# Kernel tuning notes

Hardware: AMD Instinct MI355X
Metric: run time of the kernel (lower is better)

Reference implementation:

```python
import jax, jax.numpy as jnp
import numpy as np

N, D, H = 65536, 512, 256  # batch, input_dim, hidden_dim
BN_EPS = 1e-5
EPS = 1e-15


def setup_inputs() -> dict:
    key = jax.random.key(0)
    ks = jax.random.split(key, 10)
    rn = lambda k, shape, sc: jax.random.normal(k, shape, dtype=jnp.float32) * sc
    return {
        "x1": rn(ks[0], (N, D), 1.0),
        "x2": rn(ks[1], (N, D), 1.0),
        "W1": rn(ks[2], (D, H), 0.04),
        "b1": jnp.zeros((H,), jnp.float32),
        "gamma": jnp.ones((H,), jnp.float32),
        "beta_bn": jnp.zeros((H,), jnp.float32),
        "W2": rn(ks[3], (H, H // 2), 0.06),
        "b2": jnp.zeros((H // 2,), jnp.float32),
        "W3": rn(ks[4], (H // 2 * 3, 64), 0.05),
        "b3": jnp.zeros((64,), jnp.float32),
        "W4": rn(ks[5], (64, 1), 0.12),
        "b4": jnp.zeros((1,), jnp.float32),
        "alpha": jnp.array([0.65], jnp.float32),
        "beta": jnp.array([0.25], jnp.float32),
    }


def _proj(x, W1, b1, gamma, beta_bn, W2, b2):
    h = x @ W1 + b1                       # [N, 256]
    mean = jnp.mean(h, axis=0)
    var = jnp.var(h, axis=0)              # biased, matches BN training normalization
    h = gamma * (h - mean) * jax.lax.rsqrt(var + BN_EPS) + beta_bn
    h = jax.nn.relu(h)
    return jax.nn.relu(h @ W2 + b2)       # [N, 128]


def reference(x1, x2, W1, b1, gamma, beta_bn, W2, b2, W3, b3, W4, b4, alpha, beta):
    h1 = _proj(x1, W1, b1, gamma, beta_bn, W2, b2)
    h2 = _proj(x2, W1, b1, gamma, beta_bn, W2, b2)
    # diag of normalized similarity matrix == row-wise cosine similarity
    dot = jnp.sum(h1 * h2, axis=1)
    inv1 = 1.0 / jnp.maximum(jnp.sqrt(jnp.sum(h1 * h1, axis=1)), EPS)
    inv2 = 1.0 / jnp.maximum(jnp.sqrt(jnp.sum(h2 * h2, axis=1)), EPS)
    s_math = jnp.clip(dot * inv1 * inv2, 0.0, 1.0)
    combined = jnp.concatenate([h1 * h2, jnp.abs(h1 - h2), h1 + h2], axis=1)  # [N, 384]
    s_learn = (jax.nn.relu(combined @ W3 + b3) @ W4 + b4).reshape(-1)          # [N]
    final = alpha * s_math + beta * jax.nn.sigmoid(s_learn)
    return jnp.clip(final, 0.0, 1.0)
```

## Files before the change

kernel.cpp:

```cpp
#include <hip/hip_runtime.h>
#include <hip/hip_bf16.h>
#include <math.h>

#define NROWS 65536
#define DIN   512
#define H1    256
#define H2    128
#define K3DIM 384
#define O3    64

typedef short  short8  __attribute__((ext_vector_type(8)));
typedef float  f32x4   __attribute__((ext_vector_type(4)));
typedef unsigned short u16x4 __attribute__((ext_vector_type(4)));

__device__ __forceinline__ unsigned short f2bf(float f) {
    union { float f; unsigned int i; } v; v.f = f;
    unsigned int r = (v.i + 0x7fffu + ((v.i >> 16) & 1u)) >> 16;
    return (unsigned short)r;
}
__device__ __forceinline__ float bf2f(unsigned short u) {
    union { unsigned int i; float f; } v; v.i = ((unsigned int)u) << 16;
    return v.f;
}

typedef const __attribute__((address_space(1))) unsigned int* gas1_t;
typedef __attribute__((address_space(3))) unsigned int* las3_t;
__device__ __forceinline__ void gload_lds16(const void* g, void* l) {
    __builtin_amdgcn_global_load_lds((gas1_t)g, (las3_t)l, 16, 0, 0);
}

__global__ void transpose_cvt_kernel(const float* __restrict__ src,
                                     unsigned short* __restrict__ dst, int R, int C) {
    int idx = blockIdx.x * 256 + threadIdx.x;
    if (idx >= R * C) return;
    int c = idx / R, r = idx - c * R;
    dst[idx] = f2bf(src[r * C + c]);
}

#define LDA1 32

__global__ __launch_bounds__(256, 2)
void gemm1_kernel(const float* __restrict__ x1, const float* __restrict__ x2,
                  const unsigned short* __restrict__ w1t, const float* __restrict__ b1,
                  unsigned short* __restrict__ h_out, float* __restrict__ stats) {
    __shared__ __align__(1024) unsigned short Al[64 * LDA1];
    __shared__ __align__(1024) unsigned short Bl[256 * LDA1];
    const int t    = threadIdx.x;
    const int row0 = blockIdx.x * 64;
    const int inp  = row0 >> 16;
    const float* xp = inp ? x2 : x1;
    const int r0 = row0 & (NROWS - 1);

    const int wave = t >> 6, lane = t & 63;
    const int m = lane & 15, q = lane >> 4;

    const int bn_local = lane >> 2;
    const int bk_off   = (lane & 3) * 8;

    f32x4 acc[4][4] = {};

    for (int k0 = 0; k0 < DIN; k0 += 32) {
        __syncthreads();
#pragma unroll
        for (int i = 0; i < 4; ++i) {
            int chunk = wave * 4 + i;
            int n = chunk * 16 + bn_local;
            gload_lds16(w1t + (size_t)n * DIN + k0 + bk_off, &Bl[chunk * 512]);
        }
#pragma unroll
        for (int i = 0; i < 2; ++i) {
            int u = t + i * 256;
            int r = u >> 3, kq = u & 7;
            const float4 v = *reinterpret_cast<const float4*>(xp + (size_t)(r0 + r) * DIN + k0 + kq * 4);
            u16x4 b; b.x = f2bf(v.x); b.y = f2bf(v.y); b.z = f2bf(v.z); b.w = f2bf(v.w);
            *reinterpret_cast<u16x4*>(&Al[r * LDA1 + kq * 4]) = b;
        }
        __syncthreads();
        short8 af[4], bfr[4];
#pragma unroll
        for (int mi = 0; mi < 4; ++mi)
            af[mi] = *reinterpret_cast<const short8*>(&Al[(mi * 16 + m) * LDA1 + q * 8]);
#pragma unroll
        for (int ni = 0; ni < 4; ++ni)
            bfr[ni] = *reinterpret_cast<const short8*>(&Bl[(wave * 64 + ni * 16 + m) * LDA1 + q * 8]);
#pragma unroll
        for (int mi = 0; mi < 4; ++mi)
#pragma unroll
            for (int ni = 0; ni < 4; ++ni)
                acc[mi][ni] = __builtin_amdgcn_mfma_f32_16x16x32_bf16(af[mi], bfr[ni], acc[mi][ni], 0, 0, 0);
    }

#pragma unroll
    for (int ni = 0; ni < 4; ++ni) {
        const int col = wave * 64 + ni * 16 + m;
        const float bias = b1[col];
        float s = 0.f, ssq = 0.f;
#pragma unroll
        for (int mi = 0; mi < 4; ++mi) {
#pragma unroll
            for (int r = 0; r < 4; ++r) {
                int row = row0 + mi * 16 + q * 4 + r;
                float v = acc[mi][ni][r] + bias;
                h_out[(size_t)row * H1 + col] = f2bf(v);
                s += v; ssq += v * v;
            }
        }
        s   += __shfl_xor(s, 16);   s   += __shfl_xor(s, 32);
        ssq += __shfl_xor(ssq, 16); ssq += __shfl_xor(ssq, 32);
        if (q == 0) {
            atomicAdd(&stats[(inp * 2 + 0) * H1 + col], s);
            atomicAdd(&stats[(inp * 2 + 1) * H1 + col], ssq);
        }
    }
}

__global__ void bnparams_kernel(const float* __restrict__ stats, const float* __restrict__ gamma,
                                const float* __restrict__ beta_bn, float* __restrict__ ab) {
    int t = threadIdx.x;
    int inp = t >> 8, c = t & 255;
    float mean = stats[(inp * 2 + 0) * H1 + c] * (1.0f / NROWS);
    float ex2  = stats[(inp * 2 + 1) * H1 + c] * (1.0f / NROWS);
    float var  = ex2 - mean * mean;
    float a = gamma[c] * rsqrtf(var + 1e-5f);
    ab[(inp * 2 + 0) * H1 + c] = a;
    ab[(inp * 2 + 1) * H1 + c] = beta_bn[c] - a * mean;
}

#define LDA  40
#define LDB2 264

__global__ __launch_bounds__(256, 2)
void gemm2_kernel(const unsigned short* __restrict__ h, const unsigned short* __restrict__ w2t,
                  const float* __restrict__ b2, const float* __restrict__ ab,
                  unsigned short* __restrict__ z) {
    __shared__ __align__(16) unsigned short Al[128 * LDA];
    __shared__ __align__(16) unsigned short B2[128 * LDB2];
    __shared__ float sc[H1], sh[H1];
    const int t  = threadIdx.x;
    const int m0 = blockIdx.x * 128;
    const int inp = m0 >> 16;
    if (t < 256) { sc[t] = ab[(inp * 2 + 0) * H1 + t]; sh[t] = ab[(inp * 2 + 1) * H1 + t]; }
#pragma unroll
    for (int i = 0; i < 8; ++i) {
        int c = t + i * 256;
        int n = c >> 4, kc = c & 15;
        const float4* src = reinterpret_cast<const float4*>(w2t + n * H1 + kc * 16);
        float4 v0 = src[0], v1 = src[1];
        *reinterpret_cast<float4*>(&B2[n * LDB2 + kc * 16])     = v0;
        *reinterpret_cast<float4*>(&B2[n * LDB2 + kc * 16 + 8]) = v1;
    }
    const int wave = t >> 6, lane = t & 63;
    const int wm = wave >> 1, wn = wave & 1;
    const int m = lane & 15, q = lane >> 4;
    f32x4 acc[4][4] = {};
    for (int k0 = 0; k0 < H1; k0 += 32) {
        __syncthreads();
        {
            int r = t >> 1, kh = t & 1;
            const unsigned short* src = h + (size_t)(m0 + r) * H1 + k0 + kh * 16;
            unsigned short vs[16]  __attribute__((aligned(16)));
            unsigned short ob[16]  __attribute__((aligned(16)));
            *reinterpret_cast<float4*>(vs)     = *reinterpret_cast<const float4*>(src);
            *reinterpret_cast<float4*>(vs + 8) = *reinterpret_cast<const float4*>(src + 8);
#pragma unroll
            for (int j = 0; j < 16; ++j) {
                int k = k0 + kh * 16 + j;
                float v = sc[k] * bf2f(vs[j]) + sh[k];
                ob[j] = f2bf(fmaxf(v, 0.f));
            }
            *reinterpret_cast<float4*>(&Al[r * LDA + kh * 16])     = *reinterpret_cast<float4*>(ob);
            *reinterpret_cast<float4*>(&Al[r * LDA + kh * 16 + 8]) = *reinterpret_cast<float4*>(ob + 8);
        }
        __syncthreads();
        short8 af[4], bfr[4];
#pragma unroll
        for (int mi = 0; mi < 4; ++mi)
            af[mi] = *reinterpret_cast<const short8*>(&Al[(wm * 64 + mi * 16 + m) * LDA + q * 8]);
#pragma unroll
        for (int ni = 0; ni < 4; ++ni)
            bfr[ni] = *reinterpret_cast<const short8*>(&B2[(wn * 64 + ni * 16 + m) * LDB2 + k0 + q * 8]);
#pragma unroll
        for (int mi = 0; mi < 4; ++mi)
#pragma unroll
            for (int ni = 0; ni < 4; ++ni)
                acc[mi][ni] = __builtin_amdgcn_mfma_f32_16x16x32_bf16(af[mi], bfr[ni], acc[mi][ni], 0, 0, 0);
    }
#pragma unroll
    for (int mi = 0; mi < 4; ++mi)
#pragma unroll
        for (int ni = 0; ni < 4; ++ni) {
            int col = wn * 64 + ni * 16 + m;
            float bias = b2[col];
#pragma unroll
            for (int r = 0; r < 4; ++r) {
                int row = m0 + wm * 64 + mi * 16 + q * 4 + r;
                z[(size_t)row * H2 + col] = f2bf(fmaxf(acc[mi][ni][r] + bias, 0.f));
            }
        }
}

#define LDZ  136
#define LDW3 392

__global__ __launch_bounds__(512, 2)
void head_kernel(const unsigned short* __restrict__ z, const unsigned short* __restrict__ w3t,
                 const float* __restrict__ b3, const float* __restrict__ w4,
                 const float* __restrict__ b4, const float* __restrict__ alpha,
                 const float* __restrict__ beta, float* __restrict__ out) {
    __shared__ __align__(16) unsigned short Z1[128 * LDZ];
    __shared__ __align__(16) unsigned short Z2[128 * LDZ];
    __shared__ __align__(16) unsigned short W3l[64 * LDW3];
    __shared__ float b3s[64], w4s[64];
    __shared__ float smath[128], slearn[128];

    const int t  = threadIdx.x;
    const int r0 = blockIdx.x * 128;

    {
        int r = t >> 2, seg = t & 3;
        const float4* f1 = reinterpret_cast<const float4*>(z + (size_t)(r0 + r) * H2 + seg * 32);
        const float4* f2 = reinterpret_cast<const float4*>(z + (size_t)(NROWS + r0 + r) * H2 + seg * 32);
        float4* d1 = reinterpret_cast<float4*>(&Z1[r * LDZ + seg * 32]);
        float4* d2 = reinterpret_cast<float4*>(&Z2[r * LDZ + seg * 32]);
        d1[0] = f1[0]; d1[1] = f1[1]; d1[2] = f1[2]; d1[3] = f1[3];
        d2[0] = f2[0]; d2[1] = f2[1]; d2[2] = f2[2]; d2[3] = f2[3];
    }
#pragma unroll
    for (int i = 0; i < 3; ++i) {
        int c = t + i * 512;
        int n = c / 24, kc = c - n * 24;
        const float4* src = reinterpret_cast<const float4*>(w3t + n * K3DIM + kc * 16);
        float4 v0 = src[0], v1 = src[1];
        *reinterpret_cast<float4*>(&W3l[n * LDW3 + kc * 16])     = v0;
        *reinterpret_cast<float4*>(&W3l[n * LDW3 + kc * 16 + 8]) = v1;
    }
    if (t < 64) { b3s[t] = b3[t]; w4s[t] = w4[t]; }
    __syncthreads();

    {
        int r = t >> 2, part = t & 3;
        float d = 0.f, s1 = 0.f, s2 = 0.f;
#pragma unroll
        for (int j = 0; j < 32; ++j) {
            int k = part * 32 + j;
            float a = bf2f(Z1[r * LDZ + k]);
            float b = bf2f(Z2[r * LDZ + k]);
            d += a * b; s1 += a * a; s2 += b * b;
        }
        d  += __shfl_xor(d, 1);  d  += __shfl_xor(d, 2);
        s1 += __shfl_xor(s1, 1); s1 += __shfl_xor(s1, 2);
        s2 += __shfl_xor(s2, 1); s2 += __shfl_xor(s2, 2);
        if (part == 0) {
            float inv1 = 1.f / fmaxf(sqrtf(s1), 1e-15f);
            float inv2 = 1.f / fmaxf(sqrtf(s2), 1e-15f);
            float sm = d * inv1 * inv2;
            smath[r] = fminf(fmaxf(sm, 0.f), 1.f);
        }
    }

    const int wave = t >> 6, lane = t & 63;
    const int m = lane & 15, q = lane >> 4;
    const int wr = wave * 16;
    f32x4 acc[4] = {};
#pragma unroll
    for (int kb = 0; kb < 12; ++kb) {
        int seg = kb >> 2;
        int kl  = (kb & 3) * 32 + q * 8;
        short8 a1 = *reinterpret_cast<const short8*>(&Z1[(wr + m) * LDZ + kl]);
        short8 a2 = *reinterpret_cast<const short8*>(&Z2[(wr + m) * LDZ + kl]);
        short8 af;
#pragma unroll
        for (int j = 0; j < 8; ++j) {
            float v1 = bf2f((unsigned short)a1[j]);
            float v2 = bf2f((unsigned short)a2[j]);
            float v = (seg == 0) ? v1 * v2 : (seg == 1 ? fabsf(v1 - v2) : v1 + v2);
            af[j] = (short)f2bf(v);
        }
#pragma unroll
        for (int ni = 0; ni < 4; ++ni) {
            short8 bfr = *reinterpret_cast<const short8*>(&W3l[(ni * 16 + m) * LDW3 + kb * 32 + q * 8]);
            acc[ni] = __builtin_amdgcn_mfma_f32_16x16x32_bf16(af, bfr, acc[ni], 0, 0, 0);
        }
    }
    float partial[4] = {0.f, 0.f, 0.f, 0.f};
#pragma unroll
    for (int ni = 0; ni < 4; ++ni) {
        int col = ni * 16 + m;
        float bias = b3s[col], w4v = w4s[col];
#pragma unroll
        for (int rg = 0; rg < 4; ++rg) {
            float v = fmaxf(acc[ni][rg] + bias, 0.f);
            partial[rg] += v * w4v;
        }
    }
#pragma unroll
    for (int rg = 0; rg < 4; ++rg) {
        float p = partial[rg];
        p += __shfl_xor(p, 1); p += __shfl_xor(p, 2);
        p += __shfl_xor(p, 4); p += __shfl_xor(p, 8);
        if (m == 0) slearn[wr + q * 4 + rg] = p + b4[0];
    }
    __syncthreads();
    if (t < 128) {
        float sl = slearn[t];
        float sig = 1.f / (1.f + expf(-sl));
        float f = alpha[0] * smath[t] + beta[0] * sig;
        out[r0 + t] = fminf(fmaxf(f, 0.f), 1.f);
    }
}

extern "C" void kernel_launch(void* const* d_in, const int* in_sizes, int n_in,
                              void* d_out, int out_size, void* d_ws, size_t ws_size,
                              hipStream_t stream) {
    (void)in_sizes; (void)n_in; (void)out_size; (void)ws_size;
    const float* x1      = (const float*)d_in[0];
    const float* x2      = (const float*)d_in[1];
    const float* W1      = (const float*)d_in[2];
    const float* b1      = (const float*)d_in[3];
    const float* gamma   = (const float*)d_in[4];
    const float* beta_bn = (const float*)d_in[5];
    const float* W2      = (const float*)d_in[6];
    const float* b2      = (const float*)d_in[7];
    const float* W3      = (const float*)d_in[8];
    const float* b3      = (const float*)d_in[9];
    const float* W4      = (const float*)d_in[10];
    const float* b4      = (const float*)d_in[11];
    const float* alpha   = (const float*)d_in[12];
    const float* beta    = (const float*)d_in[13];
    float* out = (float*)d_out;

    char* ws = (char*)d_ws;
    unsigned short* h   = (unsigned short*)(ws);
    unsigned short* w1t = (unsigned short*)(ws + 67108864);
    unsigned short* w2t = (unsigned short*)(ws + 67371008);
    unsigned short* w3t = (unsigned short*)(ws + 67436544);
    float*          stats = (float*)(ws + 67485696);
    float*          ab    = (float*)(ws + 67489792);
    unsigned short* z   = (unsigned short*)(ws + 67493888);

    (void)hipMemsetAsync(stats, 0, 4096, stream);
    transpose_cvt_kernel<<<(DIN * H1 + 255) / 256, 256, 0, stream>>>(W1, w1t, DIN, H1);
    transpose_cvt_kernel<<<(H1 * H2 + 255) / 256, 256, 0, stream>>>(W2, w2t, H1, H2);
    transpose_cvt_kernel<<<(K3DIM * O3 + 255) / 256, 256, 0, stream>>>(W3, w3t, K3DIM, O3);
    gemm1_kernel<<<2048, 256, 0, stream>>>(x1, x2, w1t, b1, h, stats);
    bnparams_kernel<<<1, 512, 0, stream>>>(stats, gamma, beta_bn, ab);
    gemm2_kernel<<<1024, 256, 0, stream>>>(h, w2t, b2, ab, z);
    head_kernel<<<512, 512, 0, stream>>>(z, w3t, b3, W4, b4, alpha, beta, out);
}
```

Measured before the change: 388.7 us.

## Drop LDS staging in GEMMs, load MFMA fragments directly with register double-buffering

gemm1 and gemm2 stop staging tiles in shared memory. Each wave now reads its A and B MFMA fragments straight from global memory into registers, double-buffered across k-steps, and gemm1 moves to 512-thread blocks of 128 rows. The head kernel reads W3 fragments from global instead of copying them to LDS, and the three weight-transpose launches are merged into one. This removes LDS traffic, barriers and launch overhead, but relies on L1/L2 to absorb repeated weight reads, issues less-coalesced global loads, and raises register pressure.

```diff
diff --git a/kernel.cpp b/kernel.cpp
--- a/kernel.cpp
+++ b/kernel.cpp
@@ -23,83 +23,98 @@
     return v.f;
 }
 
-typedef const __attribute__((address_space(1))) unsigned int* gas1_t;
-typedef __attribute__((address_space(3))) unsigned int* las3_t;
-__device__ __forceinline__ void gload_lds16(const void* g, void* l) {
-    __builtin_amdgcn_global_load_lds((gas1_t)g, (las3_t)l, 16, 0, 0);
-}
-
-__global__ void transpose_cvt_kernel(const float* __restrict__ src,
-                                     unsigned short* __restrict__ dst, int R, int C) {
+__global__ void transpose3_kernel(const float* __restrict__ W1, const float* __restrict__ W2,
+                                  const float* __restrict__ W3,
+                                  unsigned short* __restrict__ w1t, unsigned short* __restrict__ w2t,
+                                  unsigned short* __restrict__ w3t) {
     int idx = blockIdx.x * 256 + threadIdx.x;
-    if (idx >= R * C) return;
-    int c = idx / R, r = idx - c * R;
-    dst[idx] = f2bf(src[r * C + c]);
-}
-
-#define LDA1 32
-
-__global__ __launch_bounds__(256, 2)
+    const int n1 = DIN * H1;
+    const int n2 = H1 * H2;
+    const int n3 = K3DIM * O3;
+    if (idx < n1) {
+        int c = idx / DIN, r = idx - c * DIN;
+        w1t[idx] = f2bf(W1[r * H1 + c]);
+    } else if (idx < n1 + n2) {
+        int i2 = idx - n1;
+        int c = i2 / H1, r = i2 - c * H1;
+        w2t[i2] = f2bf(W2[r * H2 + c]);
+    } else if (idx < n1 + n2 + n3) {
+        int i3 = idx - n1 - n2;
+        int c = i3 / K3DIM, r = i3 - c * K3DIM;
+        w3t[i3] = f2bf(W3[r * O3 + c]);
+    }
+}
+
+__global__ __launch_bounds__(512, 2)
 void gemm1_kernel(const float* __restrict__ x1, const float* __restrict__ x2,
                   const unsigned short* __restrict__ w1t, const float* __restrict__ b1,
                   unsigned short* __restrict__ h_out, float* __restrict__ stats) {
-    __shared__ __align__(1024) unsigned short Al[64 * LDA1];
-    __shared__ __align__(1024) unsigned short Bl[256 * LDA1];
     const int t    = threadIdx.x;
-    const int row0 = blockIdx.x * 64;
+    const int row0 = blockIdx.x * 128;
     const int inp  = row0 >> 16;
     const float* xp = inp ? x2 : x1;
     const int r0 = row0 & (NROWS - 1);
 
-    const int wave = t >> 6, lane = t & 63;
+    const int w = t >> 6, lane = t & 63;
+    const int wr = w >> 1, wc = w & 1;
     const int m = lane & 15, q = lane >> 4;
-
-    const int bn_local = lane >> 2;
-    const int bk_off   = (lane & 3) * 8;
-
-    f32x4 acc[4][4] = {};
-
-    for (int k0 = 0; k0 < DIN; k0 += 32) {
-        __syncthreads();
-#pragma unroll
-        for (int i = 0; i < 4; ++i) {
-            int chunk = wave * 4 + i;
-            int n = chunk * 16 + bn_local;
-            gload_lds16(w1t + (size_t)n * DIN + k0 + bk_off, &Bl[chunk * 512]);
-        }
-#pragma unroll
-        for (int i = 0; i < 2; ++i) {
-            int u = t + i * 256;
-            int r = u >> 3, kq = u & 7;
-            const float4 v = *reinterpret_cast<const float4*>(xp + (size_t)(r0 + r) * DIN + k0 + kq * 4);
-            u16x4 b; b.x = f2bf(v.x); b.y = f2bf(v.y); b.z = f2bf(v.z); b.w = f2bf(v.w);
-            *reinterpret_cast<u16x4*>(&Al[r * LDA1 + kq * 4]) = b;
-        }
-        __syncthreads();
-        short8 af[4], bfr[4];
-#pragma unroll
-        for (int mi = 0; mi < 4; ++mi)
-            af[mi] = *reinterpret_cast<const short8*>(&Al[(mi * 16 + m) * LDA1 + q * 8]);
-#pragma unroll
-        for (int ni = 0; ni < 4; ++ni)
-            bfr[ni] = *reinterpret_cast<const short8*>(&Bl[(wave * 64 + ni * 16 + m) * LDA1 + q * 8]);
-#pragma unroll
-        for (int mi = 0; mi < 4; ++mi)
-#pragma unroll
-            for (int ni = 0; ni < 4; ++ni)
-                acc[mi][ni] = __builtin_amdgcn_mfma_f32_16x16x32_bf16(af[mi], bfr[ni], acc[mi][ni], 0, 0, 0);
-    }
-
-#pragma unroll
-    for (int ni = 0; ni < 4; ++ni) {
-        const int col = wave * 64 + ni * 16 + m;
+    const int rwA  = r0 + wr * 32;
+    const int col0 = wc * 128;
+
+    const float* arow0 = xp + (size_t)(rwA + m) * DIN + q * 8;
+    const float* arow1 = xp + (size_t)(rwA + 16 + m) * DIN + q * 8;
+    const unsigned short* bbase = w1t + ((size_t)col0 + m) * DIN + q * 8;
+
+    f32x4 acc[2][8] = {};
+    float4 aA0, aA1, aA2, aA3; short8 bA[8];
+    float4 aB0, aB1, aB2, aB3; short8 bB[8];
+
+#define G1_LOAD(k0, A0, A1, A2, A3, BV)                                          \
+    A0 = *reinterpret_cast<const float4*>(arow0 + (k0));                         \
+    A1 = *reinterpret_cast<const float4*>(arow0 + (k0) + 4);                     \
+    A2 = *reinterpret_cast<const float4*>(arow1 + (k0));                         \
+    A3 = *reinterpret_cast<const float4*>(arow1 + (k0) + 4);                     \
+    _Pragma("unroll")                                                            \
+    for (int ni = 0; ni < 8; ++ni)                                               \
+        BV[ni] = *reinterpret_cast<const short8*>(bbase + (size_t)ni * 16 * DIN + (k0));
+
+#define G1_COMP(A0, A1, A2, A3, BV) {                                            \
+    short8 af0, af1;                                                             \
+    af0[0]=(short)f2bf(A0.x); af0[1]=(short)f2bf(A0.y);                          \
+    af0[2]=(short)f2bf(A0.z); af0[3]=(short)f2bf(A0.w);                          \
+    af0[4]=(short)f2bf(A1.x); af0[5]=(short)f2bf(A1.y);                          \
+    af0[6]=(short)f2bf(A1.z); af0[7]=(short)f2bf(A1.w);                          \
+    af1[0]=(short)f2bf(A2.x); af1[1]=(short)f2bf(A2.y);                          \
+    af1[2]=(short)f2bf(A2.z); af1[3]=(short)f2bf(A2.w);                          \
+    af1[4]=(short)f2bf(A3.x); af1[5]=(short)f2bf(A3.y);                          \
+    af1[6]=(short)f2bf(A3.z); af1[7]=(short)f2bf(A3.w);                          \
+    _Pragma("unroll")                                                            \
+    for (int ni = 0; ni < 8; ++ni) {                                             \
+        acc[0][ni] = __builtin_amdgcn_mfma_f32_16x16x32_bf16(af0, BV[ni], acc[0][ni], 0, 0, 0); \
+        acc[1][ni] = __builtin_amdgcn_mfma_f32_16x16x32_bf16(af1, BV[ni], acc[1][ni], 0, 0, 0); \
+    } }
+
+    G1_LOAD(0, aA0, aA1, aA2, aA3, bA);
+    for (int kt2 = 0; kt2 < 8; ++kt2) {
+        const int ke = kt2 * 64;
+        G1_LOAD(ke + 32, aB0, aB1, aB2, aB3, bB);
+        G1_COMP(aA0, aA1, aA2, aA3, bA);
+        if (kt2 < 7) { G1_LOAD(ke + 64, aA0, aA1, aA2, aA3, bA); }
+        G1_COMP(aB0, aB1, aB2, aB3, bB);
+    }
+#undef G1_LOAD
+#undef G1_COMP
+
+#pragma unroll
+    for (int ni = 0; ni < 8; ++ni) {
+        const int col = col0 + ni * 16 + m;
         const float bias = b1[col];
         float s = 0.f, ssq = 0.f;
 #pragma unroll
-        for (int mi = 0; mi < 4; ++mi) {
+        for (int mi = 0; mi < 2; ++mi) {
 #pragma unroll
             for (int r = 0; r < 4; ++r) {
-                int row = row0 + mi * 16 + q * 4 + r;
+                int row = row0 + wr * 32 + mi * 16 + q * 4 + r;
                 float v = acc[mi][ni][r] + bias;
                 h_out[(size_t)row * H1 + col] = f2bf(v);
                 s += v; ssq += v * v;
@@ -126,81 +141,83 @@
     ab[(inp * 2 + 1) * H1 + c] = beta_bn[c] - a * mean;
 }
 
-#define LDA  40
-#define LDB2 264
-
 __global__ __launch_bounds__(256, 2)
 void gemm2_kernel(const unsigned short* __restrict__ h, const unsigned short* __restrict__ w2t,
                   const float* __restrict__ b2, const float* __restrict__ ab,
                   unsigned short* __restrict__ z) {
-    __shared__ __align__(16) unsigned short Al[128 * LDA];
-    __shared__ __align__(16) unsigned short B2[128 * LDB2];
-    __shared__ float sc[H1], sh[H1];
-    const int t  = threadIdx.x;
-    const int m0 = blockIdx.x * 128;
-    const int inp = m0 >> 16;
-    if (t < 256) { sc[t] = ab[(inp * 2 + 0) * H1 + t]; sh[t] = ab[(inp * 2 + 1) * H1 + t]; }
-#pragma unroll
-    for (int i = 0; i < 8; ++i) {
-        int c = t + i * 256;
-        int n = c >> 4, kc = c & 15;
-        const float4* src = reinterpret_cast<const float4*>(w2t + n * H1 + kc * 16);
-        float4 v0 = src[0], v1 = src[1];
-        *reinterpret_cast<float4*>(&B2[n * LDB2 + kc * 16])     = v0;
-        *reinterpret_cast<float4*>(&B2[n * LDB2 + kc * 16 + 8]) = v1;
-    }
-    const int wave = t >> 6, lane = t & 63;
-    const int wm = wave >> 1, wn = wave & 1;
+    const int t    = threadIdx.x;
+    const int row0 = blockIdx.x * 128;
+    const int inp  = row0 >> 16;
+    const int w = t >> 6, lane = t & 63;
     const int m = lane & 15, q = lane >> 4;
-    f32x4 acc[4][4] = {};
-    for (int k0 = 0; k0 < H1; k0 += 32) {
-        __syncthreads();
-        {
-            int r = t >> 1, kh = t & 1;
-            const unsigned short* src = h + (size_t)(m0 + r) * H1 + k0 + kh * 16;
-            unsigned short vs[16]  __attribute__((aligned(16)));
-            unsigned short ob[16]  __attribute__((aligned(16)));
-            *reinterpret_cast<float4*>(vs)     = *reinterpret_cast<const float4*>(src);
-            *reinterpret_cast<float4*>(vs + 8) = *reinterpret_cast<const float4*>(src + 8);
-#pragma unroll
-            for (int j = 0; j < 16; ++j) {
-                int k = k0 + kh * 16 + j;
-                float v = sc[k] * bf2f(vs[j]) + sh[k];
-                ob[j] = f2bf(fmaxf(v, 0.f));
-            }
-            *reinterpret_cast<float4*>(&Al[r * LDA + kh * 16])     = *reinterpret_cast<float4*>(ob);
-            *reinterpret_cast<float4*>(&Al[r * LDA + kh * 16 + 8]) = *reinterpret_cast<float4*>(ob + 8);
-        }
-        __syncthreads();
-        short8 af[4], bfr[4];
-#pragma unroll
-        for (int mi = 0; mi < 4; ++mi)
-            af[mi] = *reinterpret_cast<const short8*>(&Al[(wm * 64 + mi * 16 + m) * LDA + q * 8]);
-#pragma unroll
-        for (int ni = 0; ni < 4; ++ni)
-            bfr[ni] = *reinterpret_cast<const short8*>(&B2[(wn * 64 + ni * 16 + m) * LDB2 + k0 + q * 8]);
-#pragma unroll
-        for (int mi = 0; mi < 4; ++mi)
-#pragma unroll
-            for (int ni = 0; ni < 4; ++ni)
-                acc[mi][ni] = __builtin_amdgcn_mfma_f32_16x16x32_bf16(af[mi], bfr[ni], acc[mi][ni], 0, 0, 0);
-    }
-#pragma unroll
-    for (int mi = 0; mi < 4; ++mi)
-#pragma unroll
-        for (int ni = 0; ni < 4; ++ni) {
-            int col = wn * 64 + ni * 16 + m;
-            float bias = b2[col];
+    const int rw = row0 + w * 32;
+
+    const unsigned short* h0 = h + (size_t)(rw + m) * H1 + q * 8;
+    const unsigned short* h1 = h + (size_t)(rw + 16 + m) * H1 + q * 8;
+    const unsigned short* bbase = w2t + (size_t)m * H1 + q * 8;
+    const float* scp = ab + (inp * 2 + 0) * H1 + q * 8;
+    const float* shp = ab + (inp * 2 + 1) * H1 + q * 8;
+
+    f32x4 acc[2][8] = {};
+    short8 hA0, hA1, bA[8]; float4 scA0, scA1, shA0, shA1;
+    short8 hB0, hB1, bB[8]; float4 scB0, scB1, shB0, shB1;
+
+#define G2_LOAD(k0, H0, H1v, SC0, SC1, SH0, SH1, BV)                             \
+    H0  = *reinterpret_cast<const short8*>(h0 + (k0));                           \
+    H1v = *reinterpret_cast<const short8*>(h1 + (k0));                           \
+    SC0 = *reinterpret_cast<const float4*>(scp + (k0));                          \
+    SC1 = *reinterpret_cast<const float4*>(scp + (k0) + 4);                      \
+    SH0 = *reinterpret_cast<const float4*>(shp + (k0));                          \
+    SH1 = *reinterpret_cast<const float4*>(shp + (k0) + 4);                      \
+    _Pragma("unroll")                                                            \
+    for (int ni = 0; ni < 8; ++ni)                                               \
+        BV[ni] = *reinterpret_cast<const short8*>(bbase + (size_t)ni * 16 * H1 + (k0));
+
+#define G2_CV(u, a, b) (short)f2bf(fmaxf((a) * bf2f((unsigned short)(u)) + (b), 0.f))
+#define G2_COMP(H0, H1v, SC0, SC1, SH0, SH1, BV) {                               \
+    short8 af0, af1;                                                             \
+    af0[0]=G2_CV(H0[0],SC0.x,SH0.x); af0[1]=G2_CV(H0[1],SC0.y,SH0.y);            \
+    af0[2]=G2_CV(H0[2],SC0.z,SH0.z); af0[3]=G2_CV(H0[3],SC0.w,SH0.w);            \
+    af0[4]=G2_CV(H0[4],SC1.x,SH1.x); af0[5]=G2_CV(H0[5],SC1.y,SH1.y);            \
+    af0[6]=G2_CV(H0[6],SC1.z,SH1.z); af0[7]=G2_CV(H0[7],SC1.w,SH1.w);            \
+    af1[0]=G2_CV(H1v[0],SC0.x,SH0.x); af1[1]=G2_CV(H1v[1],SC0.y,SH0.y);          \
+    af1[2]=G2_CV(H1v[2],SC0.z,SH0.z); af1[3]=G2_CV(H1v[3],SC0.w,SH0.w);          \
+    af1[4]=G2_CV(H1v[4],SC1.x,SH1.x); af1[5]=G2_CV(H1v[5],SC1.y,SH1.y);          \
+    af1[6]=G2_CV(H1v[6],SC1.z,SH1.z); af1[7]=G2_CV(H1v[7],SC1.w,SH1.w);          \
+    _Pragma("unroll")                                                            \
+    for (int ni = 0; ni < 8; ++ni) {                                             \
+        acc[0][ni] = __builtin_amdgcn_mfma_f32_16x16x32_bf16(af0, BV[ni], acc[0][ni], 0, 0, 0); \
+        acc[1][ni] = __builtin_amdgcn_mfma_f32_16x16x32_bf16(af1, BV[ni], acc[1][ni], 0, 0, 0); \
+    } }
+
+    G2_LOAD(0, hA0, hA1, scA0, scA1, shA0, shA1, bA);
+    for (int kt2 = 0; kt2 < 4; ++kt2) {
+        const int ke = kt2 * 64;
+        G2_LOAD(ke + 32, hB0, hB1, scB0, scB1, shB0, shB1, bB);
+        G2_COMP(hA0, hA1, scA0, scA1, shA0, shA1, bA);
+        if (kt2 < 3) { G2_LOAD(ke + 64, hA0, hA1, scA0, scA1, shA0, shA1, bA); }
+        G2_COMP(hB0, hB1, scB0, scB1, shB0, shB1, bB);
+    }
+#undef G2_LOAD
+#undef G2_CV
+#undef G2_COMP
+
+#pragma unroll
+    for (int ni = 0; ni < 8; ++ni) {
+        const int col = ni * 16 + m;
+        const float bias = b2[col];
+#pragma unroll
+        for (int mi = 0; mi < 2; ++mi) {
 #pragma unroll
             for (int r = 0; r < 4; ++r) {
-                int row = m0 + wm * 64 + mi * 16 + q * 4 + r;
+                int row = rw + mi * 16 + q * 4 + r;
                 z[(size_t)row * H2 + col] = f2bf(fmaxf(acc[mi][ni][r] + bias, 0.f));
             }
         }
+    }
 }
 
 #define LDZ  136
-#define LDW3 392
 
 __global__ __launch_bounds__(512, 2)
 void head_kernel(const unsigned short* __restrict__ z, const unsigned short* __restrict__ w3t,
@@ -209,7 +226,6 @@
                  const float* __restrict__ beta, float* __restrict__ out) {
     __shared__ __align__(16) unsigned short Z1[128 * LDZ];
     __shared__ __align__(16) unsigned short Z2[128 * LDZ];
-    __shared__ __align__(16) unsigned short W3l[64 * LDW3];
     __shared__ float b3s[64], w4s[64];
     __shared__ float smath[128], slearn[128];
 
@@ -225,15 +241,6 @@
         d1[0] = f1[0]; d1[1] = f1[1]; d1[2] = f1[2]; d1[3] = f1[3];
         d2[0] = f2[0]; d2[1] = f2[1]; d2[2] = f2[2]; d2[3] = f2[3];
     }
-#pragma unroll
-    for (int i = 0; i < 3; ++i) {
-        int c = t + i * 512;
-        int n = c / 24, kc = c - n * 24;
-        const float4* src = reinterpret_cast<const float4*>(w3t + n * K3DIM + kc * 16);
-        float4 v0 = src[0], v1 = src[1];
-        *reinterpret_cast<float4*>(&W3l[n * LDW3 + kc * 16])     = v0;
-        *reinterpret_cast<float4*>(&W3l[n * LDW3 + kc * 16 + 8]) = v1;
-    }
     if (t < 64) { b3s[t] = b3[t]; w4s[t] = w4[t]; }
     __syncthreads();
 
@@ -278,7 +285,8 @@
         }
 #pragma unroll
         for (int ni = 0; ni < 4; ++ni) {
-            short8 bfr = *reinterpret_cast<const short8*>(&W3l[(ni * 16 + m) * LDW3 + kb * 32 + q * 8]);
+            short8 bfr = *reinterpret_cast<const short8*>(
+                w3t + (size_t)(ni * 16 + m) * K3DIM + kb * 32 + q * 8);
             acc[ni] = __builtin_amdgcn_mfma_f32_16x16x32_bf16(af, bfr, acc[ni], 0, 0, 0);
         }
     }
@@ -339,10 +347,9 @@
     unsigned short* z   = (unsigned short*)(ws + 67493888);
 
     (void)hipMemsetAsync(stats, 0, 4096, stream);
-    transpose_cvt_kernel<<<(DIN * H1 + 255) / 256, 256, 0, stream>>>(W1, w1t, DIN, H1);
-    transpose_cvt_kernel<<<(H1 * H2 + 255) / 256, 256, 0, stream>>>(W2, w2t, H1, H2);
-    transpose_cvt_kernel<<<(K3DIM * O3 + 255) / 256, 256, 0, stream>>>(W3, w3t, K3DIM, O3);
-    gemm1_kernel<<<2048, 256, 0, stream>>>(x1, x2, w1t, b1, h, stats);
+    transpose3_kernel<<<(DIN * H1 + H1 * H2 + K3DIM * O3 + 255) / 256, 256, 0, stream>>>(
+        W1, W2, W3, w1t, w2t, w3t);
+    gemm1_kernel<<<1024, 512, 0, stream>>>(x1, x2, w1t, b1, h, stats);
     bnparams_kernel<<<1, 512, 0, stream>>>(stats, gamma, beta_bn, ab);
     gemm2_kernel<<<1024, 256, 0, stream>>>(h, w2t, b2, ab, z);
     head_kernel<<<512, 512, 0, stream>>>(z, w3t, b3, W4, b4, alpha, beta, out);
```

Result: slower. 541.6 us (+39.3%).
